# Optimization experiments

Hardware: AMD Instinct MI355X
Metric: run time of the kernel (lower is better)

## Reference

```python
import jax, jax.numpy as jnp
import numpy as np

IN_FEATURES = 4096
OUT_FEATURES = 4096
SHARED_ROWS = 256
BATCH = 8192


def setup_inputs() -> dict:
    key = jax.random.key(0)
    k_x, k_w, k_b = jax.random.split(key, 3)
    x = jax.random.normal(k_x, (BATCH, IN_FEATURES), dtype=jnp.float32)
    shared_weights = jax.random.normal(k_w, (SHARED_ROWS, IN_FEATURES), dtype=jnp.float32)
    bias = jax.random.normal(k_b, (OUT_FEATURES,), dtype=jnp.float32)
    return {"x": x, "shared_weights": shared_weights, "bias": bias}


def reference(x, shared_weights, bias):
    # Faithful to torch: weight_matrix = shared_weights.repeat(out//shared, 1)
    reps = OUT_FEATURES // SHARED_ROWS
    weight_matrix = jnp.tile(shared_weights, (reps, 1))  # [out_features, in_features]
    # y = x @ W^T + b  -> [batch, out_features]
    return jnp.matmul(x, weight_matrix.T) + bias
```

## Files before the change

### kernel.cpp

```cpp
#include <hip/hip_runtime.h>
#include <cstdint>
#include <cstddef>

#define M_DIM 8192
#define N_DIM 256
#define K_DIM 4096
#define OUT_F 4096
#define BM 32
#define BK 64
#define LDK 72
#define S_LD 260

typedef float    float4_ __attribute__((ext_vector_type(4)));
typedef _Float16 half8   __attribute__((ext_vector_type(8)));
typedef unsigned int uint4_ __attribute__((ext_vector_type(4)));

__global__ __launch_bounds__(256) void convert_w_kernel(const float* __restrict__ w,
                                                        _Float16* __restrict__ wh) {
  int i = (blockIdx.x * 256 + threadIdx.x) * 8;
  float4_ f0 = *(const float4_*)(w + i);
  float4_ f1 = *(const float4_*)(w + i + 4);
  half8 h;
  h[0] = (_Float16)f0[0]; h[1] = (_Float16)f0[1];
  h[2] = (_Float16)f0[2]; h[3] = (_Float16)f0[3];
  h[4] = (_Float16)f1[0]; h[5] = (_Float16)f1[1];
  h[6] = (_Float16)f1[2]; h[7] = (_Float16)f1[3];
  *(half8*)(wh + i) = h;
}

__global__ __launch_bounds__(256) void swfc_kernel(const float* __restrict__ x,
                                                   const _Float16* __restrict__ wh,
                                                   const float* __restrict__ bias,
                                                   float* __restrict__ out) {
  __shared__ __align__(16) unsigned char smem[41472];
  _Float16 (*As)[LDK] = (_Float16(*)[LDK])smem;
  _Float16 (*Bs)[LDK] = (_Float16(*)[LDK])(smem + BM * LDK * 2);

  const int tid  = threadIdx.x;
  const int wv   = tid >> 6;
  const int lane = tid & 63;
  const int quad = lane >> 4;
  const int l16  = lane & 15;
  const int m0   = blockIdx.x * BM;

  const int arow = tid >> 3;
  const int acol = (tid & 7) * 8;
  const float*    xg  = x  + (size_t)(m0 + arow) * K_DIM + acol;
  const _Float16* wgb = wh + (size_t)arow * K_DIM + acol;

  float4_ acc[2][4];
  const float4_ fzero = {0.f, 0.f, 0.f, 0.f};
#pragma unroll
  for (int i = 0; i < 2; ++i)
#pragma unroll
    for (int j = 0; j < 4; ++j) acc[i][j] = fzero;

  for (int kt = 0; kt < K_DIM / BK; ++kt) {
    const int k0 = kt * BK;

    float4_ f0 = *(const float4_*)(xg + k0);
    float4_ f1 = *(const float4_*)(xg + k0 + 4);
    half8 ah;
    ah[0] = (_Float16)f0[0]; ah[1] = (_Float16)f0[1];
    ah[2] = (_Float16)f0[2]; ah[3] = (_Float16)f0[3];
    ah[4] = (_Float16)f1[0]; ah[5] = (_Float16)f1[1];
    ah[6] = (_Float16)f1[2]; ah[7] = (_Float16)f1[3];
    *(half8*)(&As[arow][acol]) = ah;

#pragma unroll
    for (int p = 0; p < 8; ++p) {
      uint4_ v = *(const uint4_*)(wgb + (size_t)p * 32 * K_DIM + k0);
      *(uint4_*)(&Bs[p * 32 + arow][acol]) = v;
    }
    __syncthreads();

#pragma unroll
    for (int ks = 0; ks < 2; ++ks) {
      const int koff = ks * 32 + quad * 8;
      half8 a0 = *(const half8*)(&As[l16][koff]);
      half8 a1 = *(const half8*)(&As[l16 + 16][koff]);
      half8 b0 = *(const half8*)(&Bs[wv * 64 + l16][koff]);
      half8 b1 = *(const half8*)(&Bs[wv * 64 + 16 + l16][koff]);
      half8 b2 = *(const half8*)(&Bs[wv * 64 + 32 + l16][koff]);
      half8 b3 = *(const half8*)(&Bs[wv * 64 + 48 + l16][koff]);
      acc[0][0] = __builtin_amdgcn_mfma_f32_16x16x32_f16(a0, b0, acc[0][0], 0, 0, 0);
      acc[1][0] = __builtin_amdgcn_mfma_f32_16x16x32_f16(a1, b0, acc[1][0], 0, 0, 0);
      acc[0][1] = __builtin_amdgcn_mfma_f32_16x16x32_f16(a0, b1, acc[0][1], 0, 0, 0);
      acc[1][1] = __builtin_amdgcn_mfma_f32_16x16x32_f16(a1, b1, acc[1][1], 0, 0, 0);
      acc[0][2] = __builtin_amdgcn_mfma_f32_16x16x32_f16(a0, b2, acc[0][2], 0, 0, 0);
      acc[1][2] = __builtin_amdgcn_mfma_f32_16x16x32_f16(a1, b2, acc[1][2], 0, 0, 0);
      acc[0][3] = __builtin_amdgcn_mfma_f32_16x16x32_f16(a0, b3, acc[0][3], 0, 0, 0);
      acc[1][3] = __builtin_amdgcn_mfma_f32_16x16x32_f16(a1, b3, acc[1][3], 0, 0, 0);
    }
    __syncthreads();
  }

  float* Sb = (float*)smem;
#pragma unroll
  for (int mf = 0; mf < 2; ++mf)
#pragma unroll
    for (int nf = 0; nf < 4; ++nf)
#pragma unroll
      for (int r = 0; r < 4; ++r)
        Sb[(mf * 16 + quad * 4 + r) * S_LD + wv * 64 + nf * 16 + l16] = acc[mf][nf][r];
  __syncthreads();

  float4_ bv[4];
  const float4_* bias4 = (const float4_*)bias;
#pragma unroll
  for (int c = 0; c < 4; ++c) bv[c] = bias4[c * 256 + tid];

  const int sc = (tid & 63) * 4;
#pragma unroll 2
  for (int m = 0; m < BM; ++m) {
    float4_ s4 = *(const float4_*)(&Sb[m * S_LD + sc]);
    float4_* orow = (float4_*)(out + (size_t)(m0 + m) * OUT_F);
#pragma unroll
    for (int c = 0; c < 4; ++c) {
      orow[c * 256 + tid] = s4 + bv[c];
    }
  }
}

extern "C" void kernel_launch(void* const* d_in, const int* in_sizes, int n_in,
                              void* d_out, int out_size, void* d_ws, size_t ws_size,
                              hipStream_t stream) {
  const float* x    = (const float*)d_in[0];
  const float* w    = (const float*)d_in[1];
  const float* bias = (const float*)d_in[2];
  float* out        = (float*)d_out;
  _Float16* wh      = (_Float16*)d_ws;

  convert_w_kernel<<<(N_DIM * K_DIM) / (256 * 8), 256, 0, stream>>>(w, wh);
  swfc_kernel<<<M_DIM / BM, 256, 0, stream>>>(x, wh, bias, out);
}
```

Baseline: 285.2 us.

## Double the block to 512 threads and register-prefetch the next K tile

Each block now runs 8 waves, and each wave computes a 32x32 output sub-tile instead of 32x64, so the block splits the same 32x256 tile across more waves. Global loads for the next K tile are issued into registers before the MFMA work on the current tile, hiding load latency behind compute. The epilogue is remapped so 512 threads each write two float4 chunks per row. The gain depends on better latency hiding through register prefetch and more waves. In exchange, each wave does fewer MFMAs per LDS A-fragment load, and the larger block with __launch_bounds__(512,2) may limit occupancy.

```diff
diff --git a/kernel.cpp b/kernel.cpp
--- a/kernel.cpp
+++ b/kernel.cpp
@@ -8,11 +8,13 @@
 #define OUT_F 4096
 #define BM 32
 #define BK 64
+#define NTH 512
 #define LDK 72
 #define S_LD 260
 
-typedef float    float4_ __attribute__((ext_vector_type(4)));
-typedef _Float16 half8   __attribute__((ext_vector_type(8)));
+typedef float    float4_  __attribute__((ext_vector_type(4)));
+typedef _Float16 half8    __attribute__((ext_vector_type(8)));
+typedef _Float16 half4    __attribute__((ext_vector_type(4)));
 typedef unsigned int uint4_ __attribute__((ext_vector_type(4)));
 
 __global__ __launch_bounds__(256) void convert_w_kernel(const float* __restrict__ w,
@@ -28,10 +30,10 @@
   *(half8*)(wh + i) = h;
 }
 
-__global__ __launch_bounds__(256) void swfc_kernel(const float* __restrict__ x,
-                                                   const _Float16* __restrict__ wh,
-                                                   const float* __restrict__ bias,
-                                                   float* __restrict__ out) {
+__global__ __launch_bounds__(512, 2) void swfc_kernel(const float* __restrict__ x,
+                                                      const _Float16* __restrict__ wh,
+                                                      const float* __restrict__ bias,
+                                                      float* __restrict__ out) {
   __shared__ __align__(16) unsigned char smem[41472];
   _Float16 (*As)[LDK] = (_Float16(*)[LDK])smem;
   _Float16 (*Bs)[LDK] = (_Float16(*)[LDK])(smem + BM * LDK * 2);
@@ -41,56 +43,58 @@
   const int lane = tid & 63;
   const int quad = lane >> 4;
   const int l16  = lane & 15;
+  const int n0   = wv * 32;
   const int m0   = blockIdx.x * BM;
 
-  const int arow = tid >> 3;
-  const int acol = (tid & 7) * 8;
-  const float*    xg  = x  + (size_t)(m0 + arow) * K_DIM + acol;
-  const _Float16* wgb = wh + (size_t)arow * K_DIM + acol;
+  const int arow = tid >> 4;
+  const int acol = (tid & 15) * 4;
+  const float* xg = x + (size_t)(m0 + arow) * K_DIM + acol;
+  const int brow = tid >> 3;
+  const int bcol = (tid & 7) * 8;
+  const _Float16* wgb = wh + (size_t)brow * K_DIM + bcol;
 
-  float4_ acc[2][4];
+  float4_ acc[2][2];
   const float4_ fzero = {0.f, 0.f, 0.f, 0.f};
 #pragma unroll
   for (int i = 0; i < 2; ++i)
 #pragma unroll
-    for (int j = 0; j < 4; ++j) acc[i][j] = fzero;
+    for (int j = 0; j < 2; ++j) acc[i][j] = fzero;
+
+  float4_ aPre = *(const float4_*)(xg);
+  uint4_ bPre[4];
+#pragma unroll
+  for (int p = 0; p < 4; ++p)
+    bPre[p] = *(const uint4_*)(wgb + (size_t)p * 64 * K_DIM);
 
   for (int kt = 0; kt < K_DIM / BK; ++kt) {
-    const int k0 = kt * BK;
+    half4 ah;
+    ah[0] = (_Float16)aPre[0]; ah[1] = (_Float16)aPre[1];
+    ah[2] = (_Float16)aPre[2]; ah[3] = (_Float16)aPre[3];
+    *(half4*)(&As[arow][acol]) = ah;
+#pragma unroll
+    for (int p = 0; p < 4; ++p)
+      *(uint4_*)(&Bs[p * 64 + brow][bcol]) = bPre[p];
+    __syncthreads();
 
-    float4_ f0 = *(const float4_*)(xg + k0);
-    float4_ f1 = *(const float4_*)(xg + k0 + 4);
-    half8 ah;
-    ah[0] = (_Float16)f0[0]; ah[1] = (_Float16)f0[1];
-    ah[2] = (_Float16)f0[2]; ah[3] = (_Float16)f0[3];
-    ah[4] = (_Float16)f1[0]; ah[5] = (_Float16)f1[1];
-    ah[6] = (_Float16)f1[2]; ah[7] = (_Float16)f1[3];
-    *(half8*)(&As[arow][acol]) = ah;
-
+    if (kt < K_DIM / BK - 1) {
+      const int k1 = (kt + 1) * BK;
+      aPre = *(const float4_*)(xg + k1);
 #pragma unroll
-    for (int p = 0; p < 8; ++p) {
-      uint4_ v = *(const uint4_*)(wgb + (size_t)p * 32 * K_DIM + k0);
-      *(uint4_*)(&Bs[p * 32 + arow][acol]) = v;
+      for (int p = 0; p < 4; ++p)
+        bPre[p] = *(const uint4_*)(wgb + (size_t)p * 64 * K_DIM + k1);
     }
-    __syncthreads();
 
 #pragma unroll
     for (int ks = 0; ks < 2; ++ks) {
       const int koff = ks * 32 + quad * 8;
       half8 a0 = *(const half8*)(&As[l16][koff]);
       half8 a1 = *(const half8*)(&As[l16 + 16][koff]);
-      half8 b0 = *(const half8*)(&Bs[wv * 64 + l16][koff]);
-      half8 b1 = *(const half8*)(&Bs[wv * 64 + 16 + l16][koff]);
-      half8 b2 = *(const half8*)(&Bs[wv * 64 + 32 + l16][koff]);
-      half8 b3 = *(const half8*)(&Bs[wv * 64 + 48 + l16][koff]);
+      half8 b0 = *(const half8*)(&Bs[n0 + l16][koff]);
+      half8 b1 = *(const half8*)(&Bs[n0 + 16 + l16][koff]);
       acc[0][0] = __builtin_amdgcn_mfma_f32_16x16x32_f16(a0, b0, acc[0][0], 0, 0, 0);
       acc[1][0] = __builtin_amdgcn_mfma_f32_16x16x32_f16(a1, b0, acc[1][0], 0, 0, 0);
       acc[0][1] = __builtin_amdgcn_mfma_f32_16x16x32_f16(a0, b1, acc[0][1], 0, 0, 0);
       acc[1][1] = __builtin_amdgcn_mfma_f32_16x16x32_f16(a1, b1, acc[1][1], 0, 0, 0);
-      acc[0][2] = __builtin_amdgcn_mfma_f32_16x16x32_f16(a0, b2, acc[0][2], 0, 0, 0);
-      acc[1][2] = __builtin_amdgcn_mfma_f32_16x16x32_f16(a1, b2, acc[1][2], 0, 0, 0);
-      acc[0][3] = __builtin_amdgcn_mfma_f32_16x16x32_f16(a0, b3, acc[0][3], 0, 0, 0);
-      acc[1][3] = __builtin_amdgcn_mfma_f32_16x16x32_f16(a1, b3, acc[1][3], 0, 0, 0);
     }
     __syncthreads();
   }
@@ -99,25 +103,25 @@
 #pragma unroll
   for (int mf = 0; mf < 2; ++mf)
 #pragma unroll
-    for (int nf = 0; nf < 4; ++nf)
+    for (int nf = 0; nf < 2; ++nf)
 #pragma unroll
       for (int r = 0; r < 4; ++r)
-        Sb[(mf * 16 + quad * 4 + r) * S_LD + wv * 64 + nf * 16 + l16] = acc[mf][nf][r];
+        Sb[(mf * 16 + quad * 4 + r) * S_LD + n0 + nf * 16 + l16] = acc[mf][nf][r];
   __syncthreads();
 
-  float4_ bv[4];
+  float4_ bv[2];
   const float4_* bias4 = (const float4_*)bias;
 #pragma unroll
-  for (int c = 0; c < 4; ++c) bv[c] = bias4[c * 256 + tid];
+  for (int c = 0; c < 2; ++c) bv[c] = bias4[c * 512 + tid];
 
   const int sc = (tid & 63) * 4;
-#pragma unroll 2
+#pragma unroll 4
   for (int m = 0; m < BM; ++m) {
     float4_ s4 = *(const float4_*)(&Sb[m * S_LD + sc]);
     float4_* orow = (float4_*)(out + (size_t)(m0 + m) * OUT_F);
 #pragma unroll
-    for (int c = 0; c < 4; ++c) {
-      orow[c * 256 + tid] = s4 + bv[c];
+    for (int c = 0; c < 2; ++c) {
+      orow[c * 512 + tid] = s4 + bv[c];
     }
   }
 }
@@ -132,5 +136,5 @@
   _Float16* wh      = (_Float16*)d_ws;
 
   convert_w_kernel<<<(N_DIM * K_DIM) / (256 * 8), 256, 0, stream>>>(w, wh);
-  swfc_kernel<<<M_DIM / BM, 256, 0, stream>>>(x, wh, bias, out);
+  swfc_kernel<<<M_DIM / BM, NTH, 0, stream>>>(x, wh, bias, out);
 }
```

Measured after the change: 278.3 us. -2.4%, faster.
